# Kernel tuning notes

Hardware: AMD Instinct MI355X
Metric: run time of the kernel (lower is better)

## Reference

```python
import jax, jax.numpy as jnp
import numpy as np

B, N, FIN, H, D = 4, 2048, 128, 4, 64
ALPHA = 0.2  # LeakyReLU negative slope


def _xavier_uniform(key, shape):
    fan_in, fan_out = shape[0], shape[1]
    limit = float(np.sqrt(6.0 / (fan_in + fan_out)))
    return jax.random.uniform(key, shape, jnp.float32, -limit, limit)


def setup_inputs() -> dict:
    key = jax.random.key(0)
    k1, k2, k3, k4 = jax.random.split(key, 4)
    x = jax.random.normal(k1, (B, N, FIN), jnp.float32)
    adj = jax.random.randint(k2, (B, N, N), 0, 2, jnp.int32)  # dense 0/1 mask
    W = _xavier_uniform(k3, (FIN, H * D))
    a = _xavier_uniform(k4, (2 * D, 1))
    return {"x": x, "adj": adj, "W": W, "a": a}


def reference(x, adj, W, a):
    Bb, Nn, _ = x.shape
    Dd = a.shape[0] // 2
    Hh = W.shape[1] // Dd
    # h: [B, N, H, D]
    h = (x @ W).reshape(Bb, Nn, Hh, Dd)
    # Additive attention: e[b,i,j,h] = leakyrelu(a1 . h[b,i,h] + a2 . h[b,j,h])
    a1 = a[:Dd, 0]
    a2 = a[Dd:, 0]
    ei = jnp.einsum('bnhd,d->bnh', h, a1)  # source (row i) term
    ej = jnp.einsum('bnhd,d->bnh', h, a2)  # dest (col j) term
    e = ei[:, :, None, :] + ej[:, None, :, :]  # [B, N, N, H]
    e = jnp.where(e >= 0, e, ALPHA * e)  # LeakyReLU
    e = jnp.where(adj[..., None] == 0, -jnp.inf, e)
    att = jax.nn.softmax(e, axis=2)  # softmax over neighbors j
    # dropout is a no-op in eval mode (training=False)
    out = jnp.einsum('bijh,bjhd->bihd', att, h)  # [B, N, H, D]
    return out.mean(axis=2)  # mean over heads -> [B, N, D]
```

## Files before the change

### kernel.cpp

```cpp
#include <hip/hip_runtime.h>

#define NN 2048
#define NH 4
#define DD 64
#define FIN 128
#define NB 4
#define LOG2E 1.44269504f

typedef unsigned short u16;
typedef unsigned int u32;
typedef short sh8 __attribute__((ext_vector_type(8)));
typedef float f32x4 __attribute__((ext_vector_type(4)));

static __device__ __forceinline__ u16 f2bf(float f) {
    u32 u = __builtin_bit_cast(u32, f);
    u += 0x7fffu + ((u >> 16) & 1u);
    return (u16)(u >> 16);
}
static __device__ __forceinline__ u32 pk_bf(float a, float b) {
    u32 ua = __builtin_bit_cast(u32, a) + 0x8000u;
    u32 ub = __builtin_bit_cast(u32, b) + 0x8000u;
    return __builtin_amdgcn_perm(ub, ua, 0x07060302u);
}
static __device__ __forceinline__ float fast_exp2(float x) {
    float r;
    asm("v_exp_f32 %0, %1" : "=v"(r) : "v"(x));
    return r;
}

static __device__ __forceinline__ void cd_probe(int ln15, int q, int* irow, int* icol) {
    sh8 pa, pb, qa, qb;
    #pragma unroll
    for (int ii = 0; ii < 8; ++ii) {
        pa[ii] = (short)f2bf((float)ln15);
        pb[ii] = 0;
        qa[ii] = 0;
        qb[ii] = (short)f2bf((float)ln15);
    }
    if (q == 0) { pb[0] = (short)f2bf(1.0f); qa[0] = (short)f2bf(1.0f); }
    f32x4 z = {};
    f32x4 prow = __builtin_amdgcn_mfma_f32_16x16x32_bf16(pa, pb, z, 0, 0, 0);
    f32x4 pcol = __builtin_amdgcn_mfma_f32_16x16x32_bf16(qa, qb, z, 0, 0, 0);
    #pragma unroll
    for (int r = 0; r < 4; ++r) {
        irow[r] = (int)(prow[r] + 0.5f);
        icol[r] = (int)(pcol[r] + 0.5f);
    }
}


__global__ __launch_bounds__(256)
void k_pack(const int* __restrict__ adj, const float* __restrict__ W,
            u32* __restrict__ msk, u16* __restrict__ WT) {
    const int tid = threadIdx.x;
    if (blockIdx.x < 2048) {
        const int wid  = (blockIdx.x * 256 + tid) >> 6;
        const int lane = tid & 63;
        for (int t = wid; t < NB * NN * 8; t += 8192) {
            const int c256 = t & 7;
            const int i    = (t >> 3) & (NN - 1);
            const int b    = t >> 14;
            const int4 v = *(const int4*)(adj + ((size_t)(b * NN + i)) * NN + c256 * 256 + lane * 4);
            u32 nib = (v.x ? 1u : 0u) | (v.y ? 2u : 0u) | (v.z ? 4u : 0u) | (v.w ? 8u : 0u);
            u32 w = nib << (4 * (lane & 7));
            w |= __shfl_xor(w, 1);
            w |= __shfl_xor(w, 2);
            w |= __shfl_xor(w, 4);
            if ((lane & 7) == 0)
                msk[((size_t)(b * 64 + c256 * 8 + (lane >> 3))) * NN + i] = w;
        }
    } else {
        const int bt  = blockIdx.x - 2048;
        const int kt  = bt & 3;
        const int ct8 = bt >> 2;
        __shared__ float tile[32][33];
        const int rr = tid >> 5, cc = tid & 31;
        #pragma unroll
        for (int i = 0; i < 4; ++i)
            tile[rr + 8 * i][cc] = W[(size_t)(kt * 32 + rr + 8 * i) * 256 + ct8 * 32 + cc];
        __syncthreads();
        #pragma unroll
        for (int i = 0; i < 4; ++i)
            WT[(size_t)(ct8 * 32 + rr + 8 * i) * FIN + kt * 32 + cc] = f2bf(tile[cc][rr + 8 * i]);
    }
}

__global__ __launch_bounds__(256)
void k_gemm_h(const float* __restrict__ x, const u16* __restrict__ WT,
              const float* __restrict__ a,
              u16* __restrict__ hTf, float* __restrict__ ei_g, float* __restrict__ ej_g) {
    const int nb = blockIdx.x, b = blockIdx.y;
    const int tid = threadIdx.x, hd = tid >> 6, lane = tid & 63, ln15 = lane & 15, q = lane >> 4;
    const int q8 = q * 8;
    const int n0 = nb * 64;

    __shared__ u16 xs[64][136];
    __shared__ float cs[NH][4][16][20];
    {
        const int col = (tid & 31) * 4;
        const int r0  = tid >> 5;
        #pragma unroll
        for (int rr = 0; rr < 8; ++rr) {
            const int row = r0 + rr * 8;
            const float4 v = *(const float4*)(x + ((size_t)(b * NN + n0 + row)) * FIN + col);
            *(u32*)&xs[row][col]     = pk_bf(v.x, v.y);
            *(u32*)&xs[row][col + 2] = pk_bf(v.z, v.w);
        }
    }
    __syncthreads();

    int irow[4], icol[4];
    cd_probe(ln15, q, irow, icol);

    f32x4 acc[4][4] = {};
    #pragma unroll
    for (int ks = 0; ks < 4; ++ks) {
        sh8 af[4], bfr[4];
        #pragma unroll
        for (int ct = 0; ct < 4; ++ct)
            af[ct] = *(const sh8*)(WT + (size_t)(hd * 64 + ct * 16 + ln15) * FIN + ks * 32 + q8);
        #pragma unroll
        for (int nt = 0; nt < 4; ++nt)
            bfr[nt] = *(const sh8*)&xs[nt * 16 + ln15][ks * 32 + q8];
        #pragma unroll
        for (int ct = 0; ct < 4; ++ct)
            #pragma unroll
            for (int nt = 0; nt < 4; ++nt)
                acc[ct][nt] = __builtin_amdgcn_mfma_f32_16x16x32_bf16(af[ct], bfr[nt], acc[ct][nt], 0, 0, 0);
    }

    float eip[4] = {}, ejq[4] = {};
    #pragma unroll
    for (int ct = 0; ct < 4; ++ct) {
        #pragma unroll
        for (int nt = 0; nt < 4; ++nt)
            #pragma unroll
            for (int r = 0; r < 4; ++r)
                cs[hd][nt][irow[r]][icol[r]] = acc[ct][nt][r];

        #pragma unroll
        for (int p = 0; p < 2; ++p) {
            const float4 c0 = *(const float4*)&cs[hd][2 * p + (q >> 1)][ln15][(q & 1) * 8];
            const float4 c1 = *(const float4*)&cs[hd][2 * p + (q >> 1)][ln15][(q & 1) * 8 + 4];
            uint4 o;
            o.x = pk_bf(c0.x, c0.y); o.y = pk_bf(c0.z, c0.w);
            o.z = pk_bf(c1.x, c1.y); o.w = pk_bf(c1.z, c1.w);
            *(uint4*)(hTf + ((((size_t)(b * NH + hd) * 64 + nb * 2 + p) * 4 + ct) * 512) + lane * 8) = o;
        }

        float a1v[4], a2v[4];
        #pragma unroll
        for (int r = 0; r < 4; ++r) {
            const int d = ct * 16 + 4 * q + r;
            a1v[r] = a[d] * LOG2E;
            a2v[r] = a[64 + d] * LOG2E;
        }
        #pragma unroll
        for (int nt = 0; nt < 4; ++nt)
            #pragma unroll
            for (int r = 0; r < 4; ++r) {
                const float v = cs[hd][nt][4 * q + r][ln15];
                eip[nt] += v * a1v[r];
                ejq[nt] += v * a2v[r];
            }
    }
    #pragma unroll
    for (int nt = 0; nt < 4; ++nt) {
        eip[nt] += __shfl_xor(eip[nt], 16);
        eip[nt] += __shfl_xor(eip[nt], 32);
        ejq[nt] += __shfl_xor(ejq[nt], 16);
        ejq[nt] += __shfl_xor(ejq[nt], 32);
    }
    if (lane < 16) {
        const size_t bhd = (size_t)(b * NH + hd) * NN;
        #pragma unroll
        for (int nt = 0; nt < 4; ++nt) {
            ei_g[bhd + n0 + nt * 16 + lane] = eip[nt];
            ej_g[bhd + n0 + nt * 16 + lane] = ejq[nt];
        }
    }
}

__global__ __launch_bounds__(256, 2)
void k_attn(const u32* __restrict__ msk, const u16* __restrict__ hTf,
            const float* __restrict__ ei_g, const float* __restrict__ ej_g,
            float* __restrict__ out) {
    const int ib = blockIdx.x, b = blockIdx.y;
    const int tid = threadIdx.x, hd = tid >> 6, lane = tid & 63, ln15 = lane & 15, q = lane >> 4;
    const int q8 = q * 8;
    const int i0 = ib * 16;

    __shared__ float o_s[NH][16][68];
    __shared__ float l_s[NH][16];

    int irow[4], icol[4];
    cd_probe(ln15, q, irow, icol);

    const size_t bhd = (size_t)(b * NH + hd) * NN;
    const float eiv = ei_g[bhd + i0 + ln15];
    const u32*   mptr = msk + (size_t)(b * 64) * NN + i0 + ln15;
    const float* ejp  = ej_g + bhd + q8;
    const u16*   hfp  = hTf + (size_t)(b * NH + hd) * (64 * 2048) + (size_t)lane * 8;

    sh8 ones;
    #pragma unroll
    for (int ii = 0; ii < 8; ++ii) ones[ii] = (short)0x3F80;

    f32x4 acc[4] = {};
    f32x4 accl = {};

    u32 m = mptr[0];
    float4 e0 = *(const float4*)(ejp);
    float4 e1 = *(const float4*)(ejp + 4);
    sh8 h0 = *(const sh8*)(hfp);
    sh8 h1 = *(const sh8*)(hfp + 512);
    sh8 h2 = *(const sh8*)(hfp + 1024);
    sh8 h3 = *(const sh8*)(hfp + 1536);

    for (int t = 0; t < 64; ++t) {
        const int tn = (t + 1) & 63;
        const u32 mn = mptr[(size_t)tn * NN];
        const float4 e0n = *(const float4*)(ejp + tn * 32);
        const float4 e1n = *(const float4*)(ejp + tn * 32 + 4);
        const sh8 h0n = *(const sh8*)(hfp + (size_t)tn * 2048);
        const sh8 h1n = *(const sh8*)(hfp + (size_t)tn * 2048 + 512);
        const sh8 h2n = *(const sh8*)(hfp + (size_t)tn * 2048 + 1024);
        const sh8 h3n = *(const sh8*)(hfp + (size_t)tn * 2048 + 1536);

        const float ef[8] = { e0.x, e0.y, e0.z, e0.w, e1.x, e1.y, e1.z, e1.w };
        const u32 mq = m >> q8;
        float p[8];
        #pragma unroll
        for (int ii = 0; ii < 8; ++ii) {
            float e = eiv + ef[ii];
            e = fmaxf(e, 0.2f * e);
            const float ex = fast_exp2(e);
            p[ii] = (mq & (1u << ii)) ? ex : 0.f;
        }
        union { uint4 u; sh8 v; } av;
        av.u.x = pk_bf(p[0], p[1]); av.u.y = pk_bf(p[2], p[3]);
        av.u.z = pk_bf(p[4], p[5]); av.u.w = pk_bf(p[6], p[7]);

        acc[0] = __builtin_amdgcn_mfma_f32_16x16x32_bf16(av.v, h0, acc[0], 0, 0, 0);
        acc[1] = __builtin_amdgcn_mfma_f32_16x16x32_bf16(av.v, h1, acc[1], 0, 0, 0);
        acc[2] = __builtin_amdgcn_mfma_f32_16x16x32_bf16(av.v, h2, acc[2], 0, 0, 0);
        acc[3] = __builtin_amdgcn_mfma_f32_16x16x32_bf16(av.v, h3, acc[3], 0, 0, 0);
        accl   = __builtin_amdgcn_mfma_f32_16x16x32_bf16(av.v, ones, accl, 0, 0, 0);

        m = mn; e0 = e0n; e1 = e1n;
        h0 = h0n; h1 = h1n; h2 = h2n; h3 = h3n;
    }

    #pragma unroll
    for (int r = 0; r < 4; ++r)
        l_s[hd][irow[r]] = accl[r];
    #pragma unroll
    for (int dt = 0; dt < 4; ++dt)
        #pragma unroll
        for (int r = 0; r < 4; ++r)
            o_s[hd][irow[r]][dt * 16 + icol[r]] = acc[dt][r];
    __syncthreads();

    {
        const int i  = tid >> 4;
        const int d4 = (tid & 15) * 4;
        float inv[NH];
        #pragma unroll
        for (int h = 0; h < NH; ++h) inv[h] = 0.25f / l_s[h][i];
        float4 s = {0.f, 0.f, 0.f, 0.f};
        #pragma unroll
        for (int h = 0; h < NH; ++h) {
            const float4 v = *(const float4*)&o_s[h][i][d4];
            s.x += v.x * inv[h]; s.y += v.y * inv[h];
            s.z += v.z * inv[h]; s.w += v.w * inv[h];
        }
        *(float4*)(out + ((size_t)(b * NN + i0 + i)) * DD + d4) = s;
    }
}

extern "C" void kernel_launch(void* const* d_in, const int* in_sizes, int n_in,
                              void* d_out, int out_size, void* d_ws, size_t ws_size,
                              hipStream_t stream) {
    const float* x = nullptr; const int* adj = nullptr;
    const float* W = nullptr; const float* a = nullptr;
    for (int i = 0; i < n_in; ++i) {
        switch (in_sizes[i]) {
            case NB * NN * FIN:  x   = (const float*)d_in[i]; break;
            case NB * NN * NN:   adj = (const int*)d_in[i];   break;
            case FIN * 256:      W   = (const float*)d_in[i]; break;
            case 2 * DD:         a   = (const float*)d_in[i]; break;
            default: break;
        }
    }
    if (!x)   x   = (const float*)d_in[0];
    if (!adj) adj = (const int*)d_in[1];
    if (!W)   W   = (const float*)d_in[2];
    if (!a)   a   = (const float*)d_in[3];
    float* out = (float*)d_out;

    char* ws = (char*)d_ws;
    u16*   hTf = (u16*)(ws);
    float* ei  = (float*)(ws + 4194304);
    float* ej  = (float*)(ws + 4325376);
    u16*   WT  = (u16*)(ws + 4456448);
    u32*   msk = (u32*)(ws + 4521984);

    k_pack<<<dim3(2080), dim3(256), 0, stream>>>(adj, W, msk, WT);
    k_gemm_h<<<dim3(32, NB), dim3(256), 0, stream>>>(x, WT, a, hTf, ei, ej);
    k_attn<<<dim3(128, NB), dim3(256), 0, stream>>>(msk, hTf, ei, ej, out);
}
```

Measured before the change: 163.9 us.

## Share h tiles across 32-row blocks via LDS DMA double buffering

The attention kernel now runs 512-thread blocks covering 32 query rows, so two wave groups per head reuse the same h tile. That tile is staged in LDS with global_load_lds into a double buffer. The ej vector and mask slice are preloaded into LDS once per block, and blocks are swizzled across batches. This roughly halves global/L2 traffic for h and removes per-lane ej and mask loads. In exchange it adds a block-wide barrier every iteration, uses about 107KB of LDS, and allows only one block per CU, which can reduce latency hiding.

```diff
diff --git a/kernel.cpp b/kernel.cpp
--- a/kernel.cpp
+++ b/kernel.cpp
@@ -26,6 +26,10 @@
     float r;
     asm("v_exp_f32 %0, %1" : "=v"(r) : "v"(x));
     return r;
+}
+static __device__ __forceinline__ void dma16(const u16* g, u16* l) {
+    __builtin_amdgcn_global_load_lds((const __attribute__((address_space(1))) void*)g,
+                                     (__attribute__((address_space(3))) void*)l, 16, 0, 0);
 }
 
 static __device__ __forceinline__ void cd_probe(int ln15, int q, int* irow, int* icol) {
@@ -181,26 +185,48 @@
     }
 }
 
-__global__ __launch_bounds__(256, 2)
+__global__ __launch_bounds__(512, 1)
 void k_attn(const u32* __restrict__ msk, const u16* __restrict__ hTf,
             const float* __restrict__ ei_g, const float* __restrict__ ej_g,
             float* __restrict__ out) {
-    const int ib = blockIdx.x, b = blockIdx.y;
-    const int tid = threadIdx.x, hd = tid >> 6, lane = tid & 63, ln15 = lane & 15, q = lane >> 4;
-    const int q8 = q * 8;
-    const int i0 = ib * 16;
-
-    __shared__ float o_s[NH][16][68];
-    __shared__ float l_s[NH][16];
+    const int bid = blockIdx.x;
+    const int b   = (bid & 7) >> 1;
+    const int ib  = ((bid >> 3) << 1) | (bid & 1);
+    const int tid = threadIdx.x;
+    const int w   = tid >> 6;
+    const int hd  = w & 3;
+    const int ih  = w >> 2;
+    const int lane = tid & 63, ln15 = lane & 15, q = lane >> 4, q8 = q * 8;
+
+    __shared__ __align__(16) u16 hbuf[2][NH][4][512];
+    __shared__ float ejs[NH][NN];
+    __shared__ u32   msk_s[64][32];
+    __shared__ float o_s[NH][32][68];
+    __shared__ float l_s[NH][32];
+
+    {
+        const int j32 = tid >> 3, ic = (tid & 7) * 4;
+        const uint4 v = *(const uint4*)(msk + ((size_t)(b * 64 + j32)) * NN + ib * 32 + ic);
+        *(uint4*)&msk_s[j32][ic] = v;
+    }
+    {
+        const int h = tid >> 7, off = (tid & 127) * 16;
+        const float* src = ej_g + (size_t)(b * NH + h) * NN + off;
+        #pragma unroll
+        for (int k = 0; k < 4; ++k)
+            *(float4*)&ejs[h][off + k * 4] = *(const float4*)(src + k * 4);
+    }
+    const u16* hfp = hTf + (size_t)(b * NH + hd) * (64 * 2048) + (size_t)lane * 8;
+    if (ih == 0) {
+        #pragma unroll
+        for (int dt = 0; dt < 4; ++dt)
+            dma16(hfp + dt * 512, &hbuf[0][hd][dt][0]);
+    }
 
     int irow[4], icol[4];
     cd_probe(ln15, q, irow, icol);
 
-    const size_t bhd = (size_t)(b * NH + hd) * NN;
-    const float eiv = ei_g[bhd + i0 + ln15];
-    const u32*   mptr = msk + (size_t)(b * 64) * NN + i0 + ln15;
-    const float* ejp  = ej_g + bhd + q8;
-    const u16*   hfp  = hTf + (size_t)(b * NH + hd) * (64 * 2048) + (size_t)lane * 8;
+    const float eiv = ei_g[(size_t)(b * NH + hd) * NN + ib * 32 + ih * 16 + ln15];
 
     sh8 ones;
     #pragma unroll
@@ -209,26 +235,26 @@
     f32x4 acc[4] = {};
     f32x4 accl = {};
 
-    u32 m = mptr[0];
-    float4 e0 = *(const float4*)(ejp);
-    float4 e1 = *(const float4*)(ejp + 4);
-    sh8 h0 = *(const sh8*)(hfp);
-    sh8 h1 = *(const sh8*)(hfp + 512);
-    sh8 h2 = *(const sh8*)(hfp + 1024);
-    sh8 h3 = *(const sh8*)(hfp + 1536);
+    __syncthreads();
 
     for (int t = 0; t < 64; ++t) {
-        const int tn = (t + 1) & 63;
-        const u32 mn = mptr[(size_t)tn * NN];
-        const float4 e0n = *(const float4*)(ejp + tn * 32);
-        const float4 e1n = *(const float4*)(ejp + tn * 32 + 4);
-        const sh8 h0n = *(const sh8*)(hfp + (size_t)tn * 2048);
-        const sh8 h1n = *(const sh8*)(hfp + (size_t)tn * 2048 + 512);
-        const sh8 h2n = *(const sh8*)(hfp + (size_t)tn * 2048 + 1024);
-        const sh8 h3n = *(const sh8*)(hfp + (size_t)tn * 2048 + 1536);
+        const int cur = t & 1, nxt = cur ^ 1;
+        if (ih == 0 && t < 63) {
+            const u16* g = hfp + (size_t)(t + 1) * 2048;
+            #pragma unroll
+            for (int dt = 0; dt < 4; ++dt)
+                dma16(g + dt * 512, &hbuf[nxt][hd][dt][0]);
+        }
+
+        const u32 mq = msk_s[t][ih * 16 + ln15] >> q8;
+        const float4 e0 = *(const float4*)&ejs[hd][t * 32 + q8];
+        const float4 e1 = *(const float4*)&ejs[hd][t * 32 + q8 + 4];
+        const sh8 h0 = *(const sh8*)&hbuf[cur][hd][0][lane * 8];
+        const sh8 h1 = *(const sh8*)&hbuf[cur][hd][1][lane * 8];
+        const sh8 h2 = *(const sh8*)&hbuf[cur][hd][2][lane * 8];
+        const sh8 h3 = *(const sh8*)&hbuf[cur][hd][3][lane * 8];
 
         const float ef[8] = { e0.x, e0.y, e0.z, e0.w, e1.x, e1.y, e1.z, e1.w };
-        const u32 mq = m >> q8;
         float p[8];
         #pragma unroll
         for (int ii = 0; ii < 8; ++ii) {
@@ -247,18 +273,17 @@
         acc[3] = __builtin_amdgcn_mfma_f32_16x16x32_bf16(av.v, h3, acc[3], 0, 0, 0);
         accl   = __builtin_amdgcn_mfma_f32_16x16x32_bf16(av.v, ones, accl, 0, 0, 0);
 
-        m = mn; e0 = e0n; e1 = e1n;
-        h0 = h0n; h1 = h1n; h2 = h2n; h3 = h3n;
+        __syncthreads();
     }
 
     #pragma unroll
     for (int r = 0; r < 4; ++r)
-        l_s[hd][irow[r]] = accl[r];
+        l_s[hd][ih * 16 + irow[r]] = accl[r];
     #pragma unroll
     for (int dt = 0; dt < 4; ++dt)
         #pragma unroll
         for (int r = 0; r < 4; ++r)
-            o_s[hd][irow[r]][dt * 16 + icol[r]] = acc[dt][r];
+            o_s[hd][ih * 16 + irow[r]][dt * 16 + icol[r]] = acc[dt][r];
     __syncthreads();
 
     {
@@ -274,7 +299,7 @@
             s.x += v.x * inv[h]; s.y += v.y * inv[h];
             s.z += v.z * inv[h]; s.w += v.w * inv[h];
         }
-        *(float4*)(out + ((size_t)(b * NN + i0 + i)) * DD + d4) = s;
+        *(float4*)(out + ((size_t)(b * NN + ib * 32 + i)) * DD + d4) = s;
     }
 }
 
@@ -307,5 +332,5 @@
 
     k_pack<<<dim3(2080), dim3(256), 0, stream>>>(adj, W, msk, WT);
     k_gemm_h<<<dim3(32, NB), dim3(256), 0, stream>>>(x, WT, a, hTf, ei, ej);
-    k_attn<<<dim3(128, NB), dim3(256), 0, stream>>>(msk, hTf, ei, ej, out);
-}
+    k_attn<<<dim3(256), dim3(512), 0, stream>>>(msk, hTf, ei, ej, out);
+}
```

Result: faster. 147.8 us (-9.8%).
